# Optimization experiments

Measured on AMD Instinct MI355X. Metric: run time of the kernel, lower is better.

The kernel has to match this reference:

```python
import jax, jax.numpy as jnp
import numpy as np

B, N, K = 4096, 16384, 512

def setup_inputs() -> dict:
    key = jax.random.key(0)
    x = jax.random.normal(key, (B, N), dtype=jnp.float32)
    return {"x": x, "k": K}

def reference(x, k):
    # Per-row abs top-k threshold + mask multiply (k < N assumed, matching config)
    Bsz = x.shape[0]
    flat = x.reshape(Bsz, -1)
    abs_flat = jnp.abs(flat)
    topk_vals, _ = jax.lax.top_k(abs_flat, k)          # [B, k]
    thresh = topk_vals[:, -1:]                          # [B, 1] kth largest abs value
    mask = (abs_flat >= thresh).astype(flat.dtype)
    return (flat * mask).reshape(x.shape)
```

## Files before the change

### kernel.cpp

```cpp
#include <hip/hip_runtime.h>

#define NT 512
#define ROWLEN 16384
#define PT 8
#define CAP 4096
#define RPB 4

typedef unsigned int u32x4 __attribute__((ext_vector_type(4)));

__device__ inline void sync_lds() {
  asm volatile("s_waitcnt lgkmcnt(0)" ::: "memory");
  __builtin_amdgcn_s_barrier();
  asm volatile("" ::: "memory");
}

__device__ inline unsigned mbcnt64(unsigned long long m) {
  unsigned lo = __builtin_amdgcn_mbcnt_lo((unsigned)m, 0u);
  return __builtin_amdgcn_mbcnt_hi((unsigned)(m >> 32), lo);
}

template<int NB>
__device__ inline void select_bin(unsigned* hist, unsigned* wtot,
                                  unsigned* sel, unsigned tid, unsigned krem) {
  constexpr int BPT = NB / NT;
  constexpr int NW = NT / 64;
  const unsigned base = tid * BPT;
  unsigned c[BPT];
  unsigned s = 0;
#pragma unroll
  for (int i = 0; i < BPT; i++) { c[i] = hist[base + i]; s += c[i]; }

  const unsigned lane = tid & 63u;
  const unsigned wid  = tid >> 6;

  unsigned suf = s;
#pragma unroll
  for (int off = 1; off < 64; off <<= 1) {
    unsigned v = __shfl_down(suf, off);
    if (lane + off < 64) suf += v;
  }
  if (lane == 0) wtot[wid] = suf;
  sync_lds();

  unsigned above = suf - s;
  for (unsigned w = wid + 1; w < NW; w++) above += wtot[w];

#pragma unroll
  for (int i = BPT - 1; i >= 0; i--) {
    unsigned cc = c[i];
    if (above < krem && above + cc >= krem) {
      sel[0] = base + (unsigned)i;
      sel[1] = krem - above;
    }
    above += cc;
  }
  sync_lds();
}

__global__ __launch_bounds__(NT, 4)
void topk_act_kernel(const float* __restrict__ x, float* __restrict__ out,
                     const int* __restrict__ kp) {
  __shared__ unsigned hist1[2048];
  __shared__ unsigned hist2[1024];
  __shared__ unsigned hist3[1024];
  __shared__ unsigned cand[CAP];
  __shared__ unsigned wtot[NT / 64];
  __shared__ unsigned sel[2];
  __shared__ unsigned cnt;

  const unsigned tid = threadIdx.x;
  const unsigned k = (unsigned)*kp;
  const size_t row0 = (size_t)blockIdx.x * RPB;

  u32x4 dA[PT], dB[PT];

  auto load_row = [&](u32x4 (&d)[PT], unsigned r) {
    const u32x4* __restrict__ xr =
        reinterpret_cast<const u32x4*>(x + (row0 + r) * (size_t)ROWLEN);
#pragma unroll
    for (int j = 0; j < PT; j++) d[j] = xr[tid + j * NT];
  };

  auto process = [&](u32x4 (&d)[PT], unsigned r) {
#pragma unroll
    for (int i = 0; i < 2048 / NT; i++) hist1[tid + i * NT] = 0u;
#pragma unroll
    for (int i = 0; i < 1024 / NT; i++) { hist2[tid + i * NT] = 0u; hist3[tid + i * NT] = 0u; }
    if (tid == 0) cnt = 0u;
    sync_lds();

#pragma unroll
    for (int j = 0; j < PT; j++) {
      atomicAdd(&hist1[(d[j].x << 1) >> 21], 1u);
      atomicAdd(&hist1[(d[j].y << 1) >> 21], 1u);
      atomicAdd(&hist1[(d[j].z << 1) >> 21], 1u);
      atomicAdd(&hist1[(d[j].w << 1) >> 21], 1u);
    }
    sync_lds();
    select_bin<2048>(hist1, wtot, sel, tid, k);
    const unsigned P1 = sel[0];
    const unsigned r1 = sel[1];

    {
      auto push = [&](unsigned a) {
        bool p = (a >> 21) == P1;
        unsigned long long m = __ballot(p);
        if (m) {
          unsigned nw = (unsigned)__popcll(m);
          if (p) {
            unsigned pre = mbcnt64(m);
            unsigned b = 0;
            if (pre == 0) b = atomicAdd(&cnt, nw);
            b = __builtin_amdgcn_readfirstlane(b);
            unsigned i = b + pre;
            if (i < CAP) cand[i] = a;
          }
        }
      };
#pragma unroll
      for (int j = 0; j < PT; j++) {
        push(d[j].x << 1); push(d[j].y << 1); push(d[j].z << 1); push(d[j].w << 1);
      }
    }
    sync_lds();
    const unsigned n = cnt;

    if (n <= CAP) {
      for (unsigned i = tid; i < n; i += NT)
        atomicAdd(&hist2[(cand[i] >> 11) & 0x3FFu], 1u);
    } else {
#pragma unroll
      for (int j = 0; j < PT; j++) {
        unsigned a;
        a = d[j].x << 1; if ((a >> 21) == P1) atomicAdd(&hist2[(a >> 11) & 0x3FFu], 1u);
        a = d[j].y << 1; if ((a >> 21) == P1) atomicAdd(&hist2[(a >> 11) & 0x3FFu], 1u);
        a = d[j].z << 1; if ((a >> 21) == P1) atomicAdd(&hist2[(a >> 11) & 0x3FFu], 1u);
        a = d[j].w << 1; if ((a >> 21) == P1) atomicAdd(&hist2[(a >> 11) & 0x3FFu], 1u);
      }
    }
    sync_lds();
    select_bin<1024>(hist2, wtot, sel, tid, r1);
    const unsigned P2 = sel[0];
    const unsigned r2 = sel[1];

    if (n <= CAP) {
      for (unsigned i = tid; i < n; i += NT) {
        unsigned a = cand[i];
        if (((a >> 11) & 0x3FFu) == P2) atomicAdd(&hist3[(a >> 1) & 0x3FFu], 1u);
      }
    } else {
      const unsigned P12 = (P1 << 10) | P2;
#pragma unroll
      for (int j = 0; j < PT; j++) {
        unsigned a;
        a = d[j].x << 1; if ((a >> 11) == P12) atomicAdd(&hist3[(a >> 1) & 0x3FFu], 1u);
        a = d[j].y << 1; if ((a >> 11) == P12) atomicAdd(&hist3[(a >> 1) & 0x3FFu], 1u);
        a = d[j].z << 1; if ((a >> 11) == P12) atomicAdd(&hist3[(a >> 1) & 0x3FFu], 1u);
        a = d[j].w << 1; if ((a >> 11) == P12) atomicAdd(&hist3[(a >> 1) & 0x3FFu], 1u);
      }
    }
    sync_lds();
    select_bin<1024>(hist3, wtot, sel, tid, r2);
    const unsigned Va = (P1 << 21) | (P2 << 11) | (sel[0] << 1);

    u32x4* __restrict__ orow =
        reinterpret_cast<u32x4*>(out + (row0 + r) * (size_t)ROWLEN);
#pragma unroll
    for (int j = 0; j < PT; j++) {
      u32x4 v = d[j];
      u32x4 o;
      o.x = ((v.x << 1) >= Va) ? v.x : 0u;
      o.y = ((v.y << 1) >= Va) ? v.y : 0u;
      o.z = ((v.z << 1) >= Va) ? v.z : 0u;
      o.w = ((v.w << 1) >= Va) ? v.w : 0u;
      __builtin_nontemporal_store(o, &orow[tid + j * NT]);
    }
  };

  load_row(dA, 0);
  load_row(dB, 1);
  process(dA, 0);
  load_row(dA, 2);
  process(dB, 1);
  load_row(dB, 3);
  process(dA, 2);
  process(dB, 3);
}

extern "C" void kernel_launch(void* const* d_in, const int* in_sizes, int n_in,
                              void* d_out, int out_size, void* d_ws, size_t ws_size,
                              hipStream_t stream) {
  const float* x   = (const float*)d_in[0];
  const int*   kp  = (const int*)d_in[1];
  float*       out = (float*)d_out;
  const int rows = out_size / ROWLEN;
  topk_act_kernel<<<rows / RPB, NT, 0, stream>>>(x, out, kp);
}
```

Measured before the change: 464.8 us.

## Use single-wave bin selection and per-lane candidate compaction with fewer block barriers

```diff
diff --git a/kernel.cpp b/kernel.cpp
--- a/kernel.cpp
+++ b/kernel.cpp
@@ -4,187 +4,197 @@
 #define ROWLEN 16384
 #define PT 8
 #define CAP 4096
-#define RPB 4
+#define RPB 2
 
 typedef unsigned int u32x4 __attribute__((ext_vector_type(4)));
 
-__device__ inline void sync_lds() {
+__device__ __forceinline__ void sync_lds() {
   asm volatile("s_waitcnt lgkmcnt(0)" ::: "memory");
   __builtin_amdgcn_s_barrier();
   asm volatile("" ::: "memory");
 }
-
-__device__ inline unsigned mbcnt64(unsigned long long m) {
-  unsigned lo = __builtin_amdgcn_mbcnt_lo((unsigned)m, 0u);
-  return __builtin_amdgcn_mbcnt_hi((unsigned)(m >> 32), lo);
+__device__ __forceinline__ void wait_lds() {
+  asm volatile("s_waitcnt lgkmcnt(0)" ::: "memory");
 }
 
 template<int NB>
-__device__ inline void select_bin(unsigned* hist, unsigned* wtot,
-                                  unsigned* sel, unsigned tid, unsigned krem) {
-  constexpr int BPT = NB / NT;
-  constexpr int NW = NT / 64;
-  const unsigned base = tid * BPT;
-  unsigned c[BPT];
+__device__ __forceinline__ void wave_select(const unsigned* hist, unsigned krem,
+                                            unsigned lane, unsigned& binOut,
+                                            unsigned& remOut) {
+  constexpr int BPL = NB / 64;
+  const unsigned base = lane * BPL;
   unsigned s = 0;
 #pragma unroll
-  for (int i = 0; i < BPT; i++) { c[i] = hist[base + i]; s += c[i]; }
-
-  const unsigned lane = tid & 63u;
-  const unsigned wid  = tid >> 6;
-
+  for (int i = 0; i < BPL; i++) s += hist[base + i];
   unsigned suf = s;
 #pragma unroll
   for (int off = 1; off < 64; off <<= 1) {
     unsigned v = __shfl_down(suf, off);
     if (lane + off < 64) suf += v;
   }
-  if (lane == 0) wtot[wid] = suf;
+  const unsigned above = suf - s;
+  unsigned pack = (above < krem && above + s >= krem)
+                      ? (0x80000000u | (lane << 24) | above) : 0u;
+#pragma unroll
+  for (int off = 1; off < 64; off <<= 1) pack |= __shfl_xor(pack, off);
+  const unsigned L      = (pack >> 24) & 63u;
+  const unsigned aboveL = pack & 0xFFFFFFu;
+
+  unsigned c2 = (lane < BPL) ? hist[L * BPL + lane] : 0u;
+  unsigned suf2 = c2;
+#pragma unroll
+  for (int off = 1; off < 64; off <<= 1) {
+    unsigned v = __shfl_down(suf2, off);
+    if (lane + off < 64) suf2 += v;
+  }
+  const unsigned above2 = aboveL + (suf2 - c2);
+  unsigned pack2 = (above2 < krem && above2 + c2 >= krem)
+                       ? (0x80000000u | (lane << 24) | (krem - above2)) : 0u;
+#pragma unroll
+  for (int off = 1; off < 64; off <<= 1) pack2 |= __shfl_xor(pack2, off);
+  binOut = L * BPL + ((pack2 >> 24) & 63u);
+  remOut = pack2 & 0xFFFFFFu;
+}
+
+__device__ __forceinline__ void process_row(
+    u32x4 (&d)[PT], unsigned k, unsigned tid, unsigned lane, unsigned wid,
+    unsigned* hist1, unsigned* hist2, unsigned* hist3, unsigned* cand,
+    unsigned* sel, unsigned* cnt, u32x4* orow) {
+#pragma unroll
+  for (int i = 0; i < 2048 / NT; i++) hist1[tid + i * NT] = 0u;
+#pragma unroll
+  for (int i = 0; i < 1024 / NT; i++) { hist2[tid + i * NT] = 0u; hist3[tid + i * NT] = 0u; }
+  if (tid == 0) *cnt = 0u;
   sync_lds();
 
-  unsigned above = suf - s;
-  for (unsigned w = wid + 1; w < NW; w++) above += wtot[w];
-
-#pragma unroll
-  for (int i = BPT - 1; i >= 0; i--) {
-    unsigned cc = c[i];
-    if (above < krem && above + cc >= krem) {
-      sel[0] = base + (unsigned)i;
-      sel[1] = krem - above;
+#pragma unroll
+  for (int j = 0; j < PT; j++) {
+    atomicAdd(&hist1[(d[j].x << 1) >> 21], 1u);
+    atomicAdd(&hist1[(d[j].y << 1) >> 21], 1u);
+    atomicAdd(&hist1[(d[j].z << 1) >> 21], 1u);
+    atomicAdd(&hist1[(d[j].w << 1) >> 21], 1u);
+  }
+  sync_lds();
+
+  unsigned P1, r1;
+  wave_select<2048>(hist1, k, lane, P1, r1);
+
+  unsigned mc = 0;
+#pragma unroll
+  for (int j = 0; j < PT; j++) {
+    mc += ((d[j].x << 1) >> 21) == P1;
+    mc += ((d[j].y << 1) >> 21) == P1;
+    mc += ((d[j].z << 1) >> 21) == P1;
+    mc += ((d[j].w << 1) >> 21) == P1;
+  }
+  unsigned pre = mc;
+#pragma unroll
+  for (int off = 1; off < 64; off <<= 1) {
+    unsigned v = __shfl_up(pre, off);
+    if (lane >= off) pre += v;
+  }
+  const unsigned wtotal = __shfl(pre, 63);
+  unsigned idx = 0;
+  if (lane == 0 && wtotal) idx = atomicAdd(cnt, wtotal);
+  idx = __builtin_amdgcn_readfirstlane(idx) + (pre - mc);
+#pragma unroll
+  for (int j = 0; j < PT; j++) {
+    unsigned a;
+    a = d[j].x << 1; if ((a >> 21) == P1) { if (idx < CAP) cand[idx] = a; idx++; }
+    a = d[j].y << 1; if ((a >> 21) == P1) { if (idx < CAP) cand[idx] = a; idx++; }
+    a = d[j].z << 1; if ((a >> 21) == P1) { if (idx < CAP) cand[idx] = a; idx++; }
+    a = d[j].w << 1; if ((a >> 21) == P1) { if (idx < CAP) cand[idx] = a; idx++; }
+  }
+  sync_lds();
+  const unsigned n = *cnt;
+
+  unsigned Va;
+  if (n <= CAP) {
+    if (wid == 0) {
+      for (unsigned i = lane; i < n; i += 64)
+        atomicAdd(&hist2[(cand[i] >> 11) & 0x3FFu], 1u);
+      wait_lds();
+      unsigned P2, r2;
+      wave_select<1024>(hist2, r1, lane, P2, r2);
+      for (unsigned i = lane; i < n; i += 64) {
+        unsigned a = cand[i];
+        if (((a >> 11) & 0x3FFu) == P2) atomicAdd(&hist3[(a >> 1) & 0x3FFu], 1u);
+      }
+      wait_lds();
+      unsigned b3, r3;
+      wave_select<1024>(hist3, r2, lane, b3, r3);
+      if (lane == 0) sel[0] = (P1 << 21) | (P2 << 11) | (b3 << 1);
     }
-    above += cc;
-  }
-  sync_lds();
-}
-
-__global__ __launch_bounds__(NT, 4)
+    sync_lds();
+    Va = sel[0];
+  } else {
+#pragma unroll
+    for (int j = 0; j < PT; j++) {
+      unsigned a;
+      a = d[j].x << 1; if ((a >> 21) == P1) atomicAdd(&hist2[(a >> 11) & 0x3FFu], 1u);
+      a = d[j].y << 1; if ((a >> 21) == P1) atomicAdd(&hist2[(a >> 11) & 0x3FFu], 1u);
+      a = d[j].z << 1; if ((a >> 21) == P1) atomicAdd(&hist2[(a >> 11) & 0x3FFu], 1u);
+      a = d[j].w << 1; if ((a >> 21) == P1) atomicAdd(&hist2[(a >> 11) & 0x3FFu], 1u);
+    }
+    sync_lds();
+    unsigned P2, r2;
+    wave_select<1024>(hist2, r1, lane, P2, r2);
+    const unsigned P12 = (P1 << 10) | P2;
+#pragma unroll
+    for (int j = 0; j < PT; j++) {
+      unsigned a;
+      a = d[j].x << 1; if ((a >> 11) == P12) atomicAdd(&hist3[(a >> 1) & 0x3FFu], 1u);
+      a = d[j].y << 1; if ((a >> 11) == P12) atomicAdd(&hist3[(a >> 1) & 0x3FFu], 1u);
+      a = d[j].z << 1; if ((a >> 11) == P12) atomicAdd(&hist3[(a >> 1) & 0x3FFu], 1u);
+      a = d[j].w << 1; if ((a >> 11) == P12) atomicAdd(&hist3[(a >> 1) & 0x3FFu], 1u);
+    }
+    sync_lds();
+    unsigned b3, r3;
+    wave_select<1024>(hist3, r2, lane, b3, r3);
+    Va = (P1 << 21) | (P2 << 11) | (b3 << 1);
+    sync_lds();
+  }
+
+#pragma unroll
+  for (int j = 0; j < PT; j++) {
+    u32x4 v = d[j], o;
+    o.x = ((v.x << 1) >= Va) ? v.x : 0u;
+    o.y = ((v.y << 1) >= Va) ? v.y : 0u;
+    o.z = ((v.z << 1) >= Va) ? v.z : 0u;
+    o.w = ((v.w << 1) >= Va) ? v.w : 0u;
+    __builtin_nontemporal_store(o, &orow[tid + j * NT]);
+  }
+}
+
+__global__ __launch_bounds__(NT)
 void topk_act_kernel(const float* __restrict__ x, float* __restrict__ out,
                      const int* __restrict__ kp) {
   __shared__ unsigned hist1[2048];
   __shared__ unsigned hist2[1024];
   __shared__ unsigned hist3[1024];
   __shared__ unsigned cand[CAP];
-  __shared__ unsigned wtot[NT / 64];
-  __shared__ unsigned sel[2];
+  __shared__ unsigned sel[1];
   __shared__ unsigned cnt;
 
   const unsigned tid = threadIdx.x;
+  const unsigned lane = tid & 63u;
+  const unsigned wid = tid >> 6;
   const unsigned k = (unsigned)*kp;
   const size_t row0 = (size_t)blockIdx.x * RPB;
 
+  const u32x4* __restrict__ xr0 = reinterpret_cast<const u32x4*>(x + row0 * (size_t)ROWLEN);
+  const u32x4* __restrict__ xr1 = reinterpret_cast<const u32x4*>(x + (row0 + 1) * (size_t)ROWLEN);
+
   u32x4 dA[PT], dB[PT];
-
-  auto load_row = [&](u32x4 (&d)[PT], unsigned r) {
-    const u32x4* __restrict__ xr =
-        reinterpret_cast<const u32x4*>(x + (row0 + r) * (size_t)ROWLEN);
-#pragma unroll
-    for (int j = 0; j < PT; j++) d[j] = xr[tid + j * NT];
-  };
-
-  auto process = [&](u32x4 (&d)[PT], unsigned r) {
-#pragma unroll
-    for (int i = 0; i < 2048 / NT; i++) hist1[tid + i * NT] = 0u;
-#pragma unroll
-    for (int i = 0; i < 1024 / NT; i++) { hist2[tid + i * NT] = 0u; hist3[tid + i * NT] = 0u; }
-    if (tid == 0) cnt = 0u;
-    sync_lds();
-
-#pragma unroll
-    for (int j = 0; j < PT; j++) {
-      atomicAdd(&hist1[(d[j].x << 1) >> 21], 1u);
-      atomicAdd(&hist1[(d[j].y << 1) >> 21], 1u);
-      atomicAdd(&hist1[(d[j].z << 1) >> 21], 1u);
-      atomicAdd(&hist1[(d[j].w << 1) >> 21], 1u);
-    }
-    sync_lds();
-    select_bin<2048>(hist1, wtot, sel, tid, k);
-    const unsigned P1 = sel[0];
-    const unsigned r1 = sel[1];
-
-    {
-      auto push = [&](unsigned a) {
-        bool p = (a >> 21) == P1;
-        unsigned long long m = __ballot(p);
-        if (m) {
-          unsigned nw = (unsigned)__popcll(m);
-          if (p) {
-            unsigned pre = mbcnt64(m);
-            unsigned b = 0;
-            if (pre == 0) b = atomicAdd(&cnt, nw);
-            b = __builtin_amdgcn_readfirstlane(b);
-            unsigned i = b + pre;
-            if (i < CAP) cand[i] = a;
-          }
-        }
-      };
-#pragma unroll
-      for (int j = 0; j < PT; j++) {
-        push(d[j].x << 1); push(d[j].y << 1); push(d[j].z << 1); push(d[j].w << 1);
-      }
-    }
-    sync_lds();
-    const unsigned n = cnt;
-
-    if (n <= CAP) {
-      for (unsigned i = tid; i < n; i += NT)
-        atomicAdd(&hist2[(cand[i] >> 11) & 0x3FFu], 1u);
-    } else {
-#pragma unroll
-      for (int j = 0; j < PT; j++) {
-        unsigned a;
-        a = d[j].x << 1; if ((a >> 21) == P1) atomicAdd(&hist2[(a >> 11) & 0x3FFu], 1u);
-        a = d[j].y << 1; if ((a >> 21) == P1) atomicAdd(&hist2[(a >> 11) & 0x3FFu], 1u);
-        a = d[j].z << 1; if ((a >> 21) == P1) atomicAdd(&hist2[(a >> 11) & 0x3FFu], 1u);
-        a = d[j].w << 1; if ((a >> 21) == P1) atomicAdd(&hist2[(a >> 11) & 0x3FFu], 1u);
-      }
-    }
-    sync_lds();
-    select_bin<1024>(hist2, wtot, sel, tid, r1);
-    const unsigned P2 = sel[0];
-    const unsigned r2 = sel[1];
-
-    if (n <= CAP) {
-      for (unsigned i = tid; i < n; i += NT) {
-        unsigned a = cand[i];
-        if (((a >> 11) & 0x3FFu) == P2) atomicAdd(&hist3[(a >> 1) & 0x3FFu], 1u);
-      }
-    } else {
-      const unsigned P12 = (P1 << 10) | P2;
-#pragma unroll
-      for (int j = 0; j < PT; j++) {
-        unsigned a;
-        a = d[j].x << 1; if ((a >> 11) == P12) atomicAdd(&hist3[(a >> 1) & 0x3FFu], 1u);
-        a = d[j].y << 1; if ((a >> 11) == P12) atomicAdd(&hist3[(a >> 1) & 0x3FFu], 1u);
-        a = d[j].z << 1; if ((a >> 11) == P12) atomicAdd(&hist3[(a >> 1) & 0x3FFu], 1u);
-        a = d[j].w << 1; if ((a >> 11) == P12) atomicAdd(&hist3[(a >> 1) & 0x3FFu], 1u);
-      }
-    }
-    sync_lds();
-    select_bin<1024>(hist3, wtot, sel, tid, r2);
-    const unsigned Va = (P1 << 21) | (P2 << 11) | (sel[0] << 1);
-
-    u32x4* __restrict__ orow =
-        reinterpret_cast<u32x4*>(out + (row0 + r) * (size_t)ROWLEN);
-#pragma unroll
-    for (int j = 0; j < PT; j++) {
-      u32x4 v = d[j];
-      u32x4 o;
-      o.x = ((v.x << 1) >= Va) ? v.x : 0u;
-      o.y = ((v.y << 1) >= Va) ? v.y : 0u;
-      o.z = ((v.z << 1) >= Va) ? v.z : 0u;
-      o.w = ((v.w << 1) >= Va) ? v.w : 0u;
-      __builtin_nontemporal_store(o, &orow[tid + j * NT]);
-    }
-  };
-
-  load_row(dA, 0);
-  load_row(dB, 1);
-  process(dA, 0);
-  load_row(dA, 2);
-  process(dB, 1);
-  load_row(dB, 3);
-  process(dA, 2);
-  process(dB, 3);
+#pragma unroll
+  for (int j = 0; j < PT; j++) dA[j] = xr0[tid + j * NT];
+#pragma unroll
+  for (int j = 0; j < PT; j++) dB[j] = xr1[tid + j * NT];
+
+  process_row(dA, k, tid, lane, wid, hist1, hist2, hist3, cand, sel, &cnt,
+              reinterpret_cast<u32x4*>(out + row0 * (size_t)ROWLEN));
+  process_row(dB, k, tid, lane, wid, hist1, hist2, hist3, cand, sel, &cnt,
+              reinterpret_cast<u32x4*>(out + (row0 + 1) * (size_t)ROWLEN));
 }
 
 extern "C" void kernel_launch(void* const* d_in, const int* in_sizes, int n_in,
```

New measurement: 509.7 us. 1.1x slower.
